# Optimization experiments

Hardware: AMD Instinct MI355X
Metric: run time of the kernel (lower is better)

## Reference

```python
import jax, jax.numpy as jnp
import numpy as np

B, T, U = 8, 200, 50
EPROJS = 512
DUNITS = 512
EMB = 512
JOINT = 512
ODIM = 1000
BLANK = 0


def setup_inputs() -> dict:
    key = jax.random.key(0)
    ks = jax.random.split(key, 16)
    s = lambda k, shape: (jax.random.normal(k, shape, jnp.float32) * 0.05)
    inp = {
        "hs_pad": jax.random.normal(ks[0], (B, T, EPROJS), jnp.float32),
        "ys_in_pad": jax.random.randint(ks[1], (B, U), 0, ODIM),
        "emb": s(ks[2], (ODIM, EMB)),
        "W_ih_0": s(ks[3], (4 * DUNITS, EMB)),
        "W_hh_0": s(ks[4], (4 * DUNITS, DUNITS)),
        "b_ih_0": s(ks[5], (4 * DUNITS,)),
        "b_hh_0": s(ks[6], (4 * DUNITS,)),
        "W_ih_1": s(ks[7], (4 * DUNITS, DUNITS)),
        "W_hh_1": s(ks[8], (4 * DUNITS, DUNITS)),
        "b_ih_1": s(ks[9], (4 * DUNITS,)),
        "b_hh_1": s(ks[10], (4 * DUNITS,)),
        "W_enc": s(ks[11], (JOINT, EPROJS)),
        "b_enc": s(ks[12], (JOINT,)),
        "W_dec": s(ks[13], (JOINT, DUNITS)),
        "W_out": s(ks[14], (ODIM, JOINT)),
        "b_out": s(ks[15], (ODIM,)),
    }
    return inp


def _lstm_cell(x, h, c, W_ih, W_hh, b_ih, b_hh):
    # torch.nn.LSTMCell, gate order i, f, g, o
    gates = x @ W_ih.T + b_ih + h @ W_hh.T + b_hh
    i, f, g, o = jnp.split(gates, 4, axis=-1)
    c_new = jax.nn.sigmoid(f) * c + jax.nn.sigmoid(i) * jnp.tanh(g)
    h_new = jax.nn.sigmoid(o) * jnp.tanh(c_new)
    return h_new, c_new


def reference(hs_pad, ys_in_pad, emb, W_ih_0, W_hh_0, b_ih_0, b_hh_0,
              W_ih_1, W_hh_1, b_ih_1, b_hh_1, W_enc, b_enc, W_dec,
              W_out, b_out):
    # embedding with padding_idx=blank -> blank row is zero
    emb_tbl = emb.at[BLANK].set(0.0)
    eys = emb_tbl[ys_in_pad]            # (B, U, EMB)

    def step(carry, ey):
        h0, c0, h1, c1 = carry
        h0, c0 = _lstm_cell(ey, h0, c0, W_ih_0, W_hh_0, b_ih_0, b_hh_0)
        h1, c1 = _lstm_cell(h0, h1, c1, W_ih_1, W_hh_1, b_ih_1, b_hh_1)
        return (h0, c0, h1, c1), h1

    z0 = jnp.zeros((hs_pad.shape[0], DUNITS), hs_pad.dtype)
    _, h_dec = jax.lax.scan(step, (z0, z0, z0, z0),
                            jnp.swapaxes(eys, 0, 1))   # (U, B, D)
    h_dec = jnp.swapaxes(h_dec, 0, 1)                  # (B, U, D)

    # joint: project first, then broadcast-add (avoids (B,T,U,Henc) expand)
    z_enc = hs_pad @ W_enc.T + b_enc                   # (B, T, J)
    z_dec = h_dec @ W_dec.T                            # (B, U, J), no bias
    z = jnp.tanh(z_enc[:, :, None, :] + z_dec[:, None, :, :])  # (B,T,U,J)
    return z @ W_out.T + b_out                         # (B, T, U, ODIM)
```

## Files before the change

kernel.cpp:

```cpp
#include <hip/hip_runtime.h>
#include <cstdint>
#include <cstddef>

#define Tsz 200
#define Usz 50
#define Kd  512
#define G4h 2048
#define OD  1000

typedef __attribute__((ext_vector_type(8))) short short8;
typedef __attribute__((ext_vector_type(4))) short s16x4;
typedef __attribute__((ext_vector_type(4))) float f32x4;

__device__ __forceinline__ unsigned short f2bf(float x) {
  union { float f; unsigned u; } v; v.f = x;
  unsigned r = v.u + 0x7FFFu + ((v.u >> 16) & 1u);
  return (unsigned short)(r >> 16);
}
__device__ __forceinline__ float bf2f(unsigned short h) {
  union { unsigned u; float f; } v; v.u = ((unsigned)h) << 16; return v.f;
}
__device__ __forceinline__ void splits(float w, short& hi, short& lo) {
  unsigned short h = f2bf(w);
  hi = (short)h;
  lo = (short)f2bf(w - bf2f(h));
}
__device__ __forceinline__ void split8(float4 f0, float4 f1, short8& hi, short8& lo) {
  float v[8] = {f0.x, f0.y, f0.z, f0.w, f1.x, f1.y, f1.z, f1.w};
  #pragma unroll
  for (int i = 0; i < 8; ++i) { short a, b2; splits(v[i], a, b2); hi[i] = a; lo[i] = b2; }
}
__device__ __forceinline__ float ftanh(float x) {
  float ax = fabsf(x);
  float t = __expf(-2.0f * ax);
  float r = (1.0f - t) / (1.0f + t);
  return copysignf(r, x);
}
__device__ __forceinline__ float sigf(float x) {
  return 1.0f / (1.0f + __expf(-x));
}
__device__ __forceinline__ void astore(unsigned* p, unsigned v) {
  __hip_atomic_store(p, v, __ATOMIC_RELAXED, __HIP_MEMORY_SCOPE_AGENT);
}
__device__ __forceinline__ void gload16(const void* g, void* l) {
  __builtin_amdgcn_global_load_lds(
      (const __attribute__((address_space(1))) void*)g,
      (__attribute__((address_space(3))) void*)l, 16, 0, 0);
}
__device__ __forceinline__ void aload4x4(const unsigned* p0, const unsigned* p1,
                                         const unsigned* p2, const unsigned* p3,
                                         uint4& r0, uint4& r1, uint4& r2, uint4& r3) {
  asm volatile(
      "global_load_dwordx4 %0, %4, off sc0 sc1\n\t"
      "global_load_dwordx4 %1, %5, off sc0 sc1\n\t"
      "global_load_dwordx4 %2, %6, off sc0 sc1\n\t"
      "global_load_dwordx4 %3, %7, off sc0 sc1\n\t"
      "s_waitcnt vmcnt(0)"
      : "=&v"(r0), "=&v"(r1), "=&v"(r2), "=&v"(r3)
      : "v"(p0), "v"(p1), "v"(p2), "v"(p3)
      : "memory");
}
__device__ __forceinline__ void aload8x4(const unsigned* p0, const unsigned* p1,
                                         const unsigned* p2, const unsigned* p3,
                                         const unsigned* q0, const unsigned* q1,
                                         const unsigned* q2, const unsigned* q3,
                                         uint4& r0, uint4& r1, uint4& r2, uint4& r3,
                                         uint4& s0, uint4& s1, uint4& s2, uint4& s3) {
  asm volatile(
      "global_load_dwordx4 %0, %8, off sc0 sc1\n\t"
      "global_load_dwordx4 %1, %9, off sc0 sc1\n\t"
      "global_load_dwordx4 %2, %10, off sc0 sc1\n\t"
      "global_load_dwordx4 %3, %11, off sc0 sc1\n\t"
      "global_load_dwordx4 %4, %12, off sc0 sc1\n\t"
      "global_load_dwordx4 %5, %13, off sc0 sc1\n\t"
      "global_load_dwordx4 %6, %14, off sc0 sc1\n\t"
      "global_load_dwordx4 %7, %15, off sc0 sc1\n\t"
      "s_waitcnt vmcnt(0)"
      : "=&v"(r0), "=&v"(r1), "=&v"(r2), "=&v"(r3),
        "=&v"(s0), "=&v"(s1), "=&v"(s2), "=&v"(s3)
      : "v"(p0), "v"(p1), "v"(p2), "v"(p3),
        "v"(q0), "v"(q1), "v"(q2), "v"(q3)
      : "memory");
}
__device__ __forceinline__ unsigned tagbad4(uint4 v, unsigned tg) {
  return ((v.x ^ tg) | (v.y ^ tg) | (v.z ^ tg) | (v.w ^ tg)) & 0xFFu;
}

__global__ __launch_bounds__(256) void k_init(unsigned* __restrict__ h0s,
                                              unsigned* __restrict__ h1s) {
  int i = blockIdx.x * 256 + threadIdx.x;
  if (i < 4096) { h0s[i] = 0u; h1s[i] = 0u; }
}

__global__ __launch_bounds__(256) void k_embed(const int* __restrict__ ys,
                                               const float* __restrict__ emb,
                                               float* __restrict__ eys) {
  int ub = blockIdx.x;
  int u = ub >> 3, b = ub & 7;
  int idx = ys[b * Usz + u];
  float* dst = eys + (size_t)ub * Kd;
  if (idx == 0) {
    for (int k = threadIdx.x; k < Kd; k += 256) dst[k] = 0.0f;
  } else {
    const float* src = emb + (size_t)idx * Kd;
    for (int k = threadIdx.x; k < Kd; k += 256) dst[k] = src[k];
  }
}

__global__ __launch_bounds__(256) void k_gemm(const float* __restrict__ A,
                                              const float* __restrict__ W,
                                              const float* __restrict__ b1,
                                              const float* __restrict__ b2,
                                              float* __restrict__ C, int N) {
  __shared__ float Al[16 * 516];
  int m0 = blockIdx.x * 16;
  int n0 = blockIdx.y * 64;
  for (int i = threadIdx.x; i < 16 * 512; i += 256) {
    int r = i >> 9, k = i & 511;
    Al[r * 516 + k] = A[(size_t)(m0 + r) * Kd + k];
  }
  __syncthreads();
  int nl = threadIdx.x & 63;
  int mg = (threadIdx.x >> 6) * 4;
  int n = n0 + nl;
  const float* Wr = W + (size_t)n * Kd;
  float acc[4] = {0.f, 0.f, 0.f, 0.f};
  #pragma unroll 4
  for (int k = 0; k < 512; k += 4) {
    float4 w = *(const float4*)(Wr + k);
    #pragma unroll
    for (int j = 0; j < 4; ++j) {
      const float* ar = &Al[(mg + j) * 516 + k];
      acc[j] += ar[0] * w.x + ar[1] * w.y + ar[2] * w.z + ar[3] * w.w;
    }
  }
  float bias = (b1 ? b1[n] : 0.0f) + (b2 ? b2[n] : 0.0f);
  #pragma unroll
  for (int j = 0; j < 4; ++j)
    C[(size_t)(m0 + mg + j) * N + n] = acc[j] + bias;
}

__global__ __launch_bounds__(256) void k_gemm_xg(const float* __restrict__ A,
                                                 const float* __restrict__ W,
                                                 const float* __restrict__ b1,
                                                 const float* __restrict__ b2,
                                                 float* __restrict__ C) {
  __shared__ float Al[16 * 516];
  int m0 = blockIdx.x * 16;
  int n0 = blockIdx.y * 64;
  for (int i = threadIdx.x; i < 16 * 512; i += 256) {
    int r = i >> 9, k = i & 511;
    Al[r * 516 + k] = A[(size_t)(m0 + r) * Kd + k];
  }
  __syncthreads();
  int nl = threadIdx.x & 63;
  int mg = (threadIdx.x >> 6) * 4;
  int n = n0 + nl;
  const float* Wr = W + (size_t)n * Kd;
  float acc[4] = {0.f, 0.f, 0.f, 0.f};
  #pragma unroll 4
  for (int k = 0; k < 512; k += 4) {
    float4 w = *(const float4*)(Wr + k);
    #pragma unroll
    for (int j = 0; j < 4; ++j) {
      const float* ar = &Al[(mg + j) * 516 + k];
      acc[j] += ar[0] * w.x + ar[1] * w.y + ar[2] * w.z + ar[3] * w.w;
    }
  }
  float bias = b1[n] + b2[n];
  int g = n >> 9, jc = n & 511;
  #pragma unroll
  for (int j = 0; j < 4; ++j) {
    int m = m0 + mg + j;
    int u = m >> 3, b = m & 7;
    C[(((size_t)u * 32 + (jc >> 4)) * 4 + g) * 128 + (jc & 15) * 8 + b] = acc[j] + bias;
  }
}

__global__ __launch_bounds__(256, 1) void k_lstm_all(
    const float* __restrict__ Whh0, const float* __restrict__ Wih1,
    const float* __restrict__ Whh1, const float* __restrict__ bih1,
    const float* __restrict__ bhh1, const float* __restrict__ xgr,
    unsigned* __restrict__ h0s, unsigned* __restrict__ h1s,
    float* __restrict__ hdec) {
  __shared__ __align__(16) unsigned short sd[34816];
  unsigned short* H0H = sd;
  unsigned short* H0L = sd + 8192;
  unsigned short* H1H = sd + 16384;
  unsigned short* H1L = sd + 24576;
  float* gsm = (float*)(sd + 32768);

  const int tid = threadIdx.x;
  const int lane = tid & 63;
  const int wv = tid >> 6;
  const int bid = blockIdx.x;
  const int kq = lane >> 4;
  const int cl = lane & 15;
  const int gg = (tid & 127) >> 1;
  const int sub = (tid & 1) << 3;
  const int swz = (gg & 7) << 4;
  const int gbase = gg << 8;
  const int tb = tid >> 7;

  if (bid < 32) {
    const int j0 = bid * 16;
    short8 whi[16], wlo[16];
    {
      const float* wr = Whh0 + ((size_t)(wv * 512 + j0 + cl)) * Kd;
      #pragma unroll
      for (int kt = 0; kt < 16; ++kt) {
        const float* p4 = wr + kt * 32 + kq * 8;
        split8(*(const float4*)p4, *(const float4*)(p4 + 4), whi[kt], wlo[kt]);
      }
    }
    float creg = 0.0f;
    const int ejl = tid & 15, eb = (tid >> 4) & 7;
    for (int p = 0; p < 50; ++p) {
      const float* xp = xgr + (((size_t)p * 32 + bid) * 4) * 128 + ejl * 8 + eb;
      float x0 = xp[0], x1 = xp[128], x2 = xp[256], x3 = xp[384];
      {
        const unsigned* bp = h0s + (size_t)p * 4096 + (tid << 2);
        uint4 v0, v1, v2, v3;
        aload4x4(bp, bp + 1024, bp + 2048, bp + 3072, v0, v1, v2, v3);
        const unsigned tg = (unsigned)p;
        for (int guard = 0; guard < (1 << 18); ++guard) {
          unsigned bad = tagbad4(v0, tg) | tagbad4(v1, tg) |
                         tagbad4(v2, tg) | tagbad4(v3, tg);
          if (!bad) break;
          __builtin_amdgcn_s_sleep(1);
          aload4x4(bp, bp + 1024, bp + 2048, bp + 3072, v0, v1, v2, v3);
        }
        unsigned uu[4][4] = {{v0.x, v0.y, v0.z, v0.w}, {v1.x, v1.y, v1.z, v1.w},
                             {v2.x, v2.y, v2.z, v2.w}, {v3.x, v3.y, v3.z, v3.w}};
        #pragma unroll
        for (int j = 0; j < 4; ++j) {
          s16x4 hv, lv;
          #pragma unroll
          for (int e = 0; e < 4; ++e) {
            short hh, ll; splits(__uint_as_float(uu[j][e]), hh, ll);
            hv[e] = hh; lv[e] = ll;
          }
          int b = j * 2 + tb;
          int off = gbase + (((b << 4) + sub) ^ swz);
          *(s16x4*)((char*)H0H + off) = hv;
          *(s16x4*)((char*)H0L + off) = lv;
        }
      }
      __syncthreads();
      f32x4 accA = {0.f, 0.f, 0.f, 0.f};
      f32x4 accB = {0.f, 0.f, 0.f, 0.f};
      f32x4 accC = {0.f, 0.f, 0.f, 0.f};
      #pragma unroll
      for (int kt = 0; kt < 16; ++kt) {
        int g = kt * 4 + kq;
        int off = (g << 8) + ((cl << 4) ^ ((g & 7) << 4));
        short8 bh = *(const short8*)((const char*)H0H + off);
        short8 bl = *(const short8*)((const char*)H0L + off);
        accA = __builtin_amdgcn_mfma_f32_16x16x32_bf16(whi[kt], bh, accA, 0, 0, 0);
        accB = __builtin_amdgcn_mfma_f32_16x16x32_bf16(wlo[kt], bh, accB, 0, 0, 0);
        accC = __builtin_amdgcn_mfma_f32_16x16x32_bf16(whi[kt], bl, accC, 0, 0, 0);
      }
      f32x4 acc = (accA + accB) + accC;
      *(f32x4*)&gsm[(wv * 16 + cl) * 16 + kq * 4] = acc;
      __syncthreads();
      if (tid < 128) {
        float g0 = gsm[(0 * 16 + eb) * 16 + ejl];
        float g1 = gsm[(1 * 16 + eb) * 16 + ejl];
        float g2 = gsm[(2 * 16 + eb) * 16 + ejl];
        float g3 = gsm[(3 * 16 + eb) * 16 + ejl];
        float gi = g0 + x0;
        float gf = g1 + x1;
        float gg2 = g2 + x2;
        float go = g3 + x3;
        float cn = sigf(gf) * creg + sigf(gi) * ftanh(gg2);
        float hn = sigf(go) * ftanh(cn);
        creg = cn;
        unsigned hv = (__float_as_uint(hn) & ~0xFFu) | (unsigned)(p + 1);
        astore(h0s + (size_t)(p + 1) * 4096 + eb * 512 + j0 + ejl, hv);
      }
      __syncthreads();
    }
  } else {
    const int j0 = (bid - 32) * 8;
    const int mt = wv & 1, kh = wv >> 1;
    short8 wihh[8], wihl[8], whhh[8], whhl[8];
    {
      const int g = mt * 2 + (cl >> 3), jl = cl & 7;
      const float* wr0 = Wih1 + ((size_t)(g * 512 + j0 + jl)) * Kd;
      const float* wr1 = Whh1 + ((size_t)(g * 512 + j0 + jl)) * Kd;
      #pragma unroll
      for (int k2 = 0; k2 < 8; ++k2) {
        int kt = kh * 8 + k2;
        const float* p0 = wr0 + kt * 32 + kq * 8;
        const float* p1 = wr1 + kt * 32 + kq * 8;
        split8(*(const float4*)p0, *(const float4*)(p0 + 4), wihh[k2], wihl[k2]);
        split8(*(const float4*)p1, *(const float4*)(p1 + 4), whhh[k2], whhl[k2]);
      }
    }
    float creg = 0.0f;
    const int ejl = tid & 7, eb = (tid >> 3) & 7;
    float bs0 = bih1[0 * 512 + j0 + ejl] + bhh1[0 * 512 + j0 + ejl];
    float bs1 = bih1[1 * 512 + j0 + ejl] + bhh1[1 * 512 + j0 + ejl];
    float bs2 = bih1[2 * 512 + j0 + ejl] + bhh1[2 * 512 + j0 + ejl];
    float bs3 = bih1[3 * 512 + j0 + ejl] + bhh1[3 * 512 + j0 + ejl];
    for (int p = 1; p <= 50; ++p) {
      {
        const unsigned* bp0 = h0s + (size_t)p * 4096 + (tid << 2);
        const unsigned* bp1 = h1s + (size_t)(p - 1) * 4096 + (tid << 2);
        uint4 v0, v1, v2, v3, w0, w1, w2, w3;
        aload8x4(bp0, bp0 + 1024, bp0 + 2048, bp0 + 3072,
                 bp1, bp1 + 1024, bp1 + 2048, bp1 + 3072,
                 v0, v1, v2, v3, w0, w1, w2, w3);
        const unsigned tg0 = (unsigned)p, tg1 = (unsigned)(p - 1);
        for (int guard = 0; guard < (1 << 18); ++guard) {
          unsigned bad = tagbad4(v0, tg0) | tagbad4(v1, tg0) |
                         tagbad4(v2, tg0) | tagbad4(v3, tg0) |
                         tagbad4(w0, tg1) | tagbad4(w1, tg1) |
                         tagbad4(w2, tg1) | tagbad4(w3, tg1);
          if (!bad) break;
          __builtin_amdgcn_s_sleep(1);
          aload8x4(bp0, bp0 + 1024, bp0 + 2048, bp0 + 3072,
                   bp1, bp1 + 1024, bp1 + 2048, bp1 + 3072,
                   v0, v1, v2, v3, w0, w1, w2, w3);
        }
        unsigned uu[4][4] = {{v0.x, v0.y, v0.z, v0.w}, {v1.x, v1.y, v1.z, v1.w},
                             {v2.x, v2.y, v2.z, v2.w}, {v3.x, v3.y, v3.z, v3.w}};
        unsigned tt[4][4] = {{w0.x, w0.y, w0.z, w0.w}, {w1.x, w1.y, w1.z, w1.w},
                             {w2.x, w2.y, w2.z, w2.w}, {w3.x, w3.y, w3.z, w3.w}};
        #pragma unroll
        for (int j = 0; j < 4; ++j) {
          s16x4 hv, lv, hw, lw;
          #pragma unroll
          for (int e = 0; e < 4; ++e) {
            short hh, ll;
            splits(__uint_as_float(uu[j][e]), hh, ll); hv[e] = hh; lv[e] = ll;
            splits(__uint_as_float(tt[j][e]), hh, ll); hw[e] = hh; lw[e] = ll;
          }
          int b = j * 2 + tb;
          int off = gbase + (((b << 4) + sub) ^ swz);
          *(s16x4*)((char*)H0H + off) = hv;
          *(s16x4*)((char*)H0L + off) = lv;
          *(s16x4*)((char*)H1H + off) = hw;
          *(s16x4*)((char*)H1L + off) = lw;
        }
      }
      __syncthreads();
      f32x4 q0 = {0.f,0.f,0.f,0.f}, q1 = {0.f,0.f,0.f,0.f}, q2 = {0.f,0.f,0.f,0.f};
      f32x4 q3 = {0.f,0.f,0.f,0.f}, q4 = {0.f,0.f,0.f,0.f}, q5 = {0.f,0.f,0.f,0.f};
      #pragma unroll
      for (int k2 = 0; k2 < 8; ++k2) {
        int kt = kh * 8 + k2;
        int g = kt * 4 + kq;
        int off = (g << 8) + ((cl << 4) ^ ((g & 7) << 4));
        short8 b0h = *(const short8*)((const char*)H0H + off);
        short8 b0l = *(const short8*)((const char*)H0L + off);
        short8 b1h = *(const short8*)((const char*)H1H + off);
        short8 b1l = *(const short8*)((const char*)H1L + off);
        q0 = __builtin_amdgcn_mfma_f32_16x16x32_bf16(wihh[k2], b0h, q0, 0, 0, 0);
        q1 = __builtin_amdgcn_mfma_f32_16x16x32_bf16(wihl[k2], b0h, q1, 0, 0, 0);
        q2 = __builtin_amdgcn_mfma_f32_16x16x32_bf16(wihh[k2], b0l, q2, 0, 0, 0);
        q3 = __builtin_amdgcn_mfma_f32_16x16x32_bf16(whhh[k2], b1h, q3, 0, 0, 0);
        q4 = __builtin_amdgcn_mfma_f32_16x16x32_bf16(whhl[k2], b1h, q4, 0, 0, 0);
        q5 = __builtin_amdgcn_mfma_f32_16x16x32_bf16(whhh[k2], b1l, q5, 0, 0, 0);
      }
      f32x4 acc = ((q0 + q1) + (q2 + q3)) + (q4 + q5);
      *(f32x4*)&gsm[(wv * 16 + cl) * 16 + kq * 4] = acc;
      __syncthreads();
      if (tid < 64) {
        float gv[4];
        #pragma unroll
        for (int g = 0; g < 4; ++g) {
          int mtg = g >> 1, r = (g & 1) * 8 + ejl;
          gv[g] = gsm[(mtg * 16 + eb) * 16 + r] + gsm[((2 + mtg) * 16 + eb) * 16 + r];
        }
        float gi = gv[0] + bs0, gf = gv[1] + bs1, gg2 = gv[2] + bs2, go = gv[3] + bs3;
        float cn = sigf(gf) * creg + sigf(gi) * ftanh(gg2);
        float hn = sigf(go) * ftanh(cn);
        creg = cn;
        int jg = j0 + ejl;
        unsigned hv = (__float_as_uint(hn) & ~0xFFu) | (unsigned)p;
        astore(h1s + (size_t)p * 4096 + eb * 512 + jg, hv);
        hdec[((size_t)eb * Usz + (p - 1)) * Kd + jg] = __uint_as_float(hv);
      }
      __syncthreads();
    }
  }
}

__global__ __launch_bounds__(256) void k_wcvt(const float* __restrict__ W,
                                              unsigned short* __restrict__ Wb) {
  int idx = blockIdx.x * 256 + threadIdx.x;
  int n = idx >> 6, chunk = idx & 63;
  short8 v;
  if (n < OD) {
    const float* src = W + (size_t)n * Kd + chunk * 8;
    #pragma unroll
    for (int j = 0; j < 8; ++j) v[j] = (short)f2bf(src[j]);
  } else {
    #pragma unroll
    for (int j = 0; j < 8; ++j) v[j] = 0;
  }
  int tile = n >> 5, srow = n & 31;
  size_t off = (size_t)tile * 32768 + srow * 1024 + ((chunk * 16) ^ ((srow & 7) << 4));
  *(short8*)((char*)Wb + off) = v;
}

__global__ __launch_bounds__(256) void k_joint(const float* __restrict__ zenc,
                                               const float* __restrict__ zdec,
                                               const unsigned short* __restrict__ Wb,
                                               const float* __restrict__ bout,
                                               float* __restrict__ out) {
  __shared__ __align__(16) unsigned short Blds[2 * 16384];
  const int lane = threadIdx.x & 63;
  const int wv = threadIdx.x >> 6;
  const int kgrp = lane >> 4;
  const int rl = lane & 15;

  for (int item = blockIdx.x; item < 1250; item += 512) {
    const int rbase = item * 64 + wv * 16;

    short8 a[16];
    {
      int row = rbase + rl;
      int u = row % Usz;
      int bt = row / Usz;
      const float* ze = zenc + (size_t)bt * Kd;
      const float* zd = zdec + (size_t)((bt / Tsz) * Usz + u) * Kd;
      #pragma unroll
      for (int kk = 0; kk < 16; ++kk) {
        int k0 = kk * 32 + kgrp * 8;
        float4 e0 = *(const float4*)(ze + k0);
        float4 e1 = *(const float4*)(ze + k0 + 4);
        float4 d0 = *(const float4*)(zd + k0);
        float4 d1 = *(const float4*)(zd + k0 + 4);
        short8 tt;
        tt[0] = (short)f2bf(ftanh(e0.x + d0.x));
        tt[1] = (short)f2bf(ftanh(e0.y + d0.y));
        tt[2] = (short)f2bf(ftanh(e0.z + d0.z));
        tt[3] = (short)f2bf(ftanh(e0.w + d0.w));
        tt[4] = (short)f2bf(ftanh(e1.x + d1.x));
        tt[5] = (short)f2bf(ftanh(e1.y + d1.y));
        tt[6] = (short)f2bf(ftanh(e1.z + d1.z));
        tt[7] = (short)f2bf(ftanh(e1.w + d1.w));
        a[kk] = tt;
      }
    }

    #pragma unroll
    for (int i = 0; i < 8; ++i) {
      int o = (i * 4 + wv) * 1024;
      gload16((const char*)Wb + o + lane * 16, (char*)Blds + o);
    }
    __syncthreads();

    int cur = 0;
    for (int it = 0; it < 32; ++it) {
      if (it < 31) {
        const char* g = (const char*)Wb + (size_t)(it + 1) * 32768;
        char* l = (char*)Blds + (cur ^ 1) * 32768;
        #pragma unroll
        for (int i = 0; i < 8; ++i) {
          int o = (i * 4 + wv) * 1024;
          gload16(g + o + lane * 16, l + o);
        }
      }
      const char* bufc = (const char*)Blds + cur * 32768;
      int n0 = it * 32;
      f32x4 acc0 = {0.f, 0.f, 0.f, 0.f};
      f32x4 acc1 = {0.f, 0.f, 0.f, 0.f};
      #pragma unroll
      for (int kk = 0; kk < 16; ++kk) {
        int c = kk * 4 + kgrp;
        int b0 = ((c * 16) ^ ((rl & 7) << 4)) + rl * 1024;
        int b1 = ((c * 16) ^ ((rl & 7) << 4)) + (rl + 16) * 1024;
        short8 bf0 = *(const short8*)(bufc + b0);
        short8 bf1 = *(const short8*)(bufc + b1);
        acc0 = __builtin_amdgcn_mfma_f32_16x16x32_bf16(a[kk], bf0, acc0, 0, 0, 0);
        acc1 = __builtin_amdgcn_mfma_f32_16x16x32_bf16(a[kk], bf1, acc1, 0, 0, 0);
      }
      #pragma unroll
      for (int nt = 0; nt < 2; ++nt) {
        int n = n0 + nt * 16 + rl;
        if (n < OD) {
          float bo = bout[n];
          const f32x4& A0 = nt ? acc1 : acc0;
          size_t r0 = (size_t)(rbase + kgrp * 4) * OD + n;
          #pragma unroll
          for (int j = 0; j < 4; ++j)
            out[r0 + (size_t)j * OD] = A0[j] + bo;
        }
      }
      __syncthreads();
      cur ^= 1;
    }
  }
}

extern "C" void kernel_launch(void* const* d_in, const int* in_sizes, int n_in,
                              void* d_out, int out_size, void* d_ws, size_t ws_size,
                              hipStream_t stream) {
  const float* hs   = (const float*)d_in[0];
  const int*   ys   = (const int*)d_in[1];
  const float* emb  = (const float*)d_in[2];
  const float* Wih0 = (const float*)d_in[3];
  const float* Whh0 = (const float*)d_in[4];
  const float* bih0 = (const float*)d_in[5];
  const float* bhh0 = (const float*)d_in[6];
  const float* Wih1 = (const float*)d_in[7];
  const float* Whh1 = (const float*)d_in[8];
  const float* bih1 = (const float*)d_in[9];
  const float* bhh1 = (const float*)d_in[10];
  const float* Wenc = (const float*)d_in[11];
  const float* benc = (const float*)d_in[12];
  const float* Wdec = (const float*)d_in[13];
  const float* Wout = (const float*)d_in[14];
  const float* bout = (const float*)d_in[15];
  float* out = (float*)d_out;

  float* ws   = (float*)d_ws;
  float* eys  = ws;
  float* xgr  = ws + 204800;
  float* zenc = ws + 1024000;
  float* zdec = ws + 1843200;
  float* hdec = ws + 2048000;
  unsigned short* Wb = (unsigned short*)(ws + 2252800);
  unsigned* h0s = (unsigned*)(ws + 2514944);
  unsigned* h1s = (unsigned*)(ws + 2723840);

  k_init<<<16, 256, 0, stream>>>(h0s, h1s);
  k_embed<<<400, 256, 0, stream>>>(ys, emb, eys);
  k_gemm_xg<<<dim3(25, 32), 256, 0, stream>>>(eys, Wih0, bih0, bhh0, xgr);
  k_gemm<<<dim3(100, 8), 256, 0, stream>>>(hs, Wenc, benc, nullptr, zenc, 512);
  k_wcvt<<<256, 256, 0, stream>>>(Wout, Wb);
  k_lstm_all<<<96, 256, 0, stream>>>(Whh0, Wih1, Whh1, bih1, bhh1, xgr,
                                     h0s, h1s, hdec);
  k_gemm<<<dim3(25, 8), 256, 0, stream>>>(hdec, Wdec, nullptr, nullptr, zdec, 512);
  k_joint<<<512, 256, 0, stream>>>(zenc, zdec, Wb, bout, out);
}
```

Before: 437.2 us.

## Merge prep kernels into one launch and retune joint pipeline sync

```diff
diff --git a/kernel.cpp b/kernel.cpp
--- a/kernel.cpp
+++ b/kernel.cpp
@@ -86,31 +86,116 @@
   return ((v.x ^ tg) | (v.y ^ tg) | (v.z ^ tg) | (v.w ^ tg)) & 0xFFu;
 }
 
-__global__ __launch_bounds__(256) void k_init(unsigned* __restrict__ h0s,
-                                              unsigned* __restrict__ h1s) {
-  int i = blockIdx.x * 256 + threadIdx.x;
-  if (i < 4096) { h0s[i] = 0u; h1s[i] = 0u; }
-}
-
-__global__ __launch_bounds__(256) void k_embed(const int* __restrict__ ys,
-                                               const float* __restrict__ emb,
-                                               float* __restrict__ eys) {
-  int ub = blockIdx.x;
-  int u = ub >> 3, b = ub & 7;
-  int idx = ys[b * Usz + u];
-  float* dst = eys + (size_t)ub * Kd;
-  if (idx == 0) {
-    for (int k = threadIdx.x; k < Kd; k += 256) dst[k] = 0.0f;
-  } else {
-    const float* src = emb + (size_t)idx * Kd;
-    for (int k = threadIdx.x; k < Kd; k += 256) dst[k] = src[k];
+__global__ __launch_bounds__(256) void k_prep(
+    const int* __restrict__ ys, const float* __restrict__ emb,
+    const float* __restrict__ Wih0, const float* __restrict__ bih0,
+    const float* __restrict__ bhh0, const float* __restrict__ hs,
+    const float* __restrict__ Wenc, const float* __restrict__ benc,
+    const float* __restrict__ Wout,
+    unsigned* __restrict__ h0s, unsigned* __restrict__ h1s,
+    unsigned short* __restrict__ Wb, float* __restrict__ zenc,
+    float* __restrict__ xgr) {
+  __shared__ float Al[16 * 516];
+  __shared__ int idxs[16];
+  const int bid = blockIdx.x;
+  const int tid = threadIdx.x;
+
+  if (bid < 16) {
+    int i = bid * 256 + tid;
+    if (i < 4096) { h0s[i] = 0u; h1s[i] = 0u; }
+    return;
+  }
+  if (bid < 272) {
+    int idx = (bid - 16) * 256 + tid;
+    int n = idx >> 6, chunk = idx & 63;
+    short8 v;
+    if (n < OD) {
+      const float* src = Wout + (size_t)n * Kd + chunk * 8;
+      #pragma unroll
+      for (int j = 0; j < 8; ++j) v[j] = (short)f2bf(src[j]);
+    } else {
+      #pragma unroll
+      for (int j = 0; j < 8; ++j) v[j] = 0;
+    }
+    int tile = n >> 5, srow = n & 31;
+    size_t off = (size_t)tile * 32768 + srow * 1024 +
+                 ((chunk * 16) ^ ((srow & 7) << 4));
+    *(short8*)((char*)Wb + off) = v;
+    return;
+  }
+  if (bid < 1072) {
+    int q = bid - 272;
+    int m0 = (q % 100) * 16;
+    int n0 = (q / 100) * 64;
+    for (int i = tid; i < 16 * 512; i += 256) {
+      int r = i >> 9, k = i & 511;
+      Al[r * 516 + k] = hs[(size_t)(m0 + r) * Kd + k];
+    }
+    __syncthreads();
+    int nl = tid & 63;
+    int mg = (tid >> 6) * 4;
+    int n = n0 + nl;
+    const float* Wr = Wenc + (size_t)n * Kd;
+    float acc[4] = {0.f, 0.f, 0.f, 0.f};
+    #pragma unroll 4
+    for (int k = 0; k < 512; k += 4) {
+      float4 w = *(const float4*)(Wr + k);
+      #pragma unroll
+      for (int j = 0; j < 4; ++j) {
+        const float* ar = &Al[(mg + j) * 516 + k];
+        acc[j] += ar[0] * w.x + ar[1] * w.y + ar[2] * w.z + ar[3] * w.w;
+      }
+    }
+    float bias = benc[n];
+    #pragma unroll
+    for (int j = 0; j < 4; ++j)
+      zenc[(size_t)(m0 + mg + j) * 512 + n] = acc[j] + bias;
+    return;
+  }
+  {
+    int q = bid - 1072;
+    int m0 = (q % 25) * 16;
+    int n0 = (q / 25) * 64;
+    if (tid < 16) {
+      int m = m0 + tid;
+      int u = m >> 3, b = m & 7;
+      idxs[tid] = ys[b * Usz + u];
+    }
+    __syncthreads();
+    for (int i = tid; i < 16 * 512; i += 256) {
+      int r = i >> 9, k = i & 511;
+      int idx = idxs[r];
+      Al[r * 516 + k] = (idx == 0) ? 0.0f : emb[(size_t)idx * Kd + k];
+    }
+    __syncthreads();
+    int nl = tid & 63;
+    int mg = (tid >> 6) * 4;
+    int n = n0 + nl;
+    const float* Wr = Wih0 + (size_t)n * Kd;
+    float acc[4] = {0.f, 0.f, 0.f, 0.f};
+    #pragma unroll 4
+    for (int k = 0; k < 512; k += 4) {
+      float4 w = *(const float4*)(Wr + k);
+      #pragma unroll
+      for (int j = 0; j < 4; ++j) {
+        const float* ar = &Al[(mg + j) * 516 + k];
+        acc[j] += ar[0] * w.x + ar[1] * w.y + ar[2] * w.z + ar[3] * w.w;
+      }
+    }
+    float bias = bih0[n] + bhh0[n];
+    int g = n >> 9, jc = n & 511;
+    #pragma unroll
+    for (int j = 0; j < 4; ++j) {
+      int m = m0 + mg + j;
+      int u = m >> 3, b = m & 7;
+      xgr[(((size_t)u * 32 + (jc >> 4)) * 4 + g) * 128 + (jc & 15) * 8 + b] =
+          acc[j] + bias;
+    }
   }
 }
 
 __global__ __launch_bounds__(256) void k_gemm(const float* __restrict__ A,
                                               const float* __restrict__ W,
-                                              const float* __restrict__ b1,
-                                              const float* __restrict__ b2,
                                               float* __restrict__ C, int N) {
   __shared__ float Al[16 * 516];
   int m0 = blockIdx.x * 16;
@@ -134,47 +219,9 @@
       acc[j] += ar[0] * w.x + ar[1] * w.y + ar[2] * w.z + ar[3] * w.w;
     }
   }
-  float bias = (b1 ? b1[n] : 0.0f) + (b2 ? b2[n] : 0.0f);
   #pragma unroll
   for (int j = 0; j < 4; ++j)
-    C[(size_t)(m0 + mg + j) * N + n] = acc[j] + bias;
-}
-
-__global__ __launch_bounds__(256) void k_gemm_xg(const float* __restrict__ A,
-                                                 const float* __restrict__ W,
-                                                 const float* __restrict__ b1,
-                                                 const float* __restrict__ b2,
-                                                 float* __restrict__ C) {
-  __shared__ float Al[16 * 516];
-  int m0 = blockIdx.x * 16;
-  int n0 = blockIdx.y * 64;
-  for (int i = threadIdx.x; i < 16 * 512; i += 256) {
-    int r = i >> 9, k = i & 511;
-    Al[r * 516 + k] = A[(size_t)(m0 + r) * Kd + k];
-  }
-  __syncthreads();
-  int nl = threadIdx.x & 63;
-  int mg = (threadIdx.x >> 6) * 4;
-  int n = n0 + nl;
-  const float* Wr = W + (size_t)n * Kd;
-  float acc[4] = {0.f, 0.f, 0.f, 0.f};
-  #pragma unroll 4
-  for (int k = 0; k < 512; k += 4) {
-    float4 w = *(const float4*)(Wr + k);
-    #pragma unroll
-    for (int j = 0; j < 4; ++j) {
-      const float* ar = &Al[(mg + j) * 516 + k];
-      acc[j] += ar[0] * w.x + ar[1] * w.y + ar[2] * w.z + ar[3] * w.w;
-    }
-  }
-  float bias = b1[n] + b2[n];
-  int g = n >> 9, jc = n & 511;
-  #pragma unroll
-  for (int j = 0; j < 4; ++j) {
-    int m = m0 + mg + j;
-    int u = m >> 3, b = m & 7;
-    C[(((size_t)u * 32 + (jc >> 4)) * 4 + g) * 128 + (jc & 15) * 8 + b] = acc[j] + bias;
-  }
+    C[(size_t)(m0 + mg + j) * N + n] = acc[j];
 }
 
 __global__ __launch_bounds__(256, 1) void k_lstm_all(
@@ -387,24 +434,6 @@
   }
 }
 
-__global__ __launch_bounds__(256) void k_wcvt(const float* __restrict__ W,
-                                              unsigned short* __restrict__ Wb) {
-  int idx = blockIdx.x * 256 + threadIdx.x;
-  int n = idx >> 6, chunk = idx & 63;
-  short8 v;
-  if (n < OD) {
-    const float* src = W + (size_t)n * Kd + chunk * 8;
-    #pragma unroll
-    for (int j = 0; j < 8; ++j) v[j] = (short)f2bf(src[j]);
-  } else {
-    #pragma unroll
-    for (int j = 0; j < 8; ++j) v[j] = 0;
-  }
-  int tile = n >> 5, srow = n & 31;
-  size_t off = (size_t)tile * 32768 + srow * 1024 + ((chunk * 16) ^ ((srow & 7) << 4));
-  *(short8*)((char*)Wb + off) = v;
-}
-
 __global__ __launch_bounds__(256) void k_joint(const float* __restrict__ zenc,
                                                const float* __restrict__ zdec,
                                                const unsigned short* __restrict__ Wb,
@@ -415,84 +444,89 @@
   const int wv = threadIdx.x >> 6;
   const int kgrp = lane >> 4;
   const int rl = lane & 15;
-
-  for (int item = blockIdx.x; item < 1250; item += 512) {
-    const int rbase = item * 64 + wv * 16;
-
-    short8 a[16];
-    {
-      int row = rbase + rl;
-      int u = row % Usz;
-      int bt = row / Usz;
-      const float* ze = zenc + (size_t)bt * Kd;
-      const float* zd = zdec + (size_t)((bt / Tsz) * Usz + u) * Kd;
-      #pragma unroll
-      for (int kk = 0; kk < 16; ++kk) {
-        int k0 = kk * 32 + kgrp * 8;
-        float4 e0 = *(const float4*)(ze + k0);
-        float4 e1 = *(const float4*)(ze + k0 + 4);
-        float4 d0 = *(const float4*)(zd + k0);
-        float4 d1 = *(const float4*)(zd + k0 + 4);
-        short8 tt;
-        tt[0] = (short)f2bf(ftanh(e0.x + d0.x));
-        tt[1] = (short)f2bf(ftanh(e0.y + d0.y));
-        tt[2] = (short)f2bf(ftanh(e0.z + d0.z));
-        tt[3] = (short)f2bf(ftanh(e0.w + d0.w));
-        tt[4] = (short)f2bf(ftanh(e1.x + d1.x));
-        tt[5] = (short)f2bf(ftanh(e1.y + d1.y));
-        tt[6] = (short)f2bf(ftanh(e1.z + d1.z));
-        tt[7] = (short)f2bf(ftanh(e1.w + d1.w));
-        a[kk] = tt;
-      }
-    }
-
+  const int rbase = blockIdx.x * 64 + wv * 16;
+
+  short8 a[16];
+  {
+    int row = rbase + rl;
+    int u = row % Usz;
+    int bt = row / Usz;
+    const float* ze = zenc + (size_t)bt * Kd;
+    const float* zd = zdec + (size_t)((bt / Tsz) * Usz + u) * Kd;
     #pragma unroll
-    for (int i = 0; i < 8; ++i) {
-      int o = (i * 4 + wv) * 1024;
-      gload16((const char*)Wb + o + lane * 16, (char*)Blds + o);
-    }
-    __syncthreads();
-
-    int cur = 0;
-    for (int it = 0; it < 32; ++it) {
-      if (it < 31) {
-        const char* g = (const char*)Wb + (size_t)(it + 1) * 32768;
-        char* l = (char*)Blds + (cur ^ 1) * 32768;
+    for (int kk = 0; kk < 16; ++kk) {
+      int k0 = kk * 32 + kgrp * 8;
+      float4 e0 = *(const float4*)(ze + k0);
+      float4 e1 = *(const float4*)(ze + k0 + 4);
+      float4 d0 = *(const float4*)(zd + k0);
+      float4 d1 = *(const float4*)(zd + k0 + 4);
+      short8 tt;
+      tt[0] = (short)f2bf(ftanh(e0.x + d0.x));
+      tt[1] = (short)f2bf(ftanh(e0.y + d0.y));
+      tt[2] = (short)f2bf(ftanh(e0.z + d0.z));
+      tt[3] = (short)f2bf(ftanh(e0.w + d0.w));
+      tt[4] = (short)f2bf(ftanh(e1.x + d1.x));
+      tt[5] = (short)f2bf(ftanh(e1.y + d1.y));
+      tt[6] = (short)f2bf(ftanh(e1.z + d1.z));
+      tt[7] = (short)f2bf(ftanh(e1.w + d1.w));
+      a[kk] = tt;
+    }
+  }
+
+  #pragma unroll
+  for (int i = 0; i < 8; ++i) {
+    int o = (i * 4 + wv) * 1024;
+    gload16((const char*)Wb + o + lane * 16, (char*)Blds + o);
+  }
+  asm volatile("s_waitcnt vmcnt(0)" ::: "memory");
+  __builtin_amdgcn_s_barrier();
+  __builtin_amdgcn_sched_barrier(0);
+
+  int cur = 0;
+  for (int it = 0; it < 32; ++it) {
+    if (it < 31) {
+      const char* g = (const char*)Wb + (size_t)(it + 1) * 32768;
+      char* l = (char*)Blds + (cur ^ 1) * 32768;
+      #pragma unroll
+      for (int i = 0; i < 8; ++i) {
+        int o = (i * 4 + wv) * 1024;
+        gload16(g + o + lane * 16, l + o);
+      }
+      __builtin_amdgcn_sched_barrier(0);
+    }
+    const char* bufc = (const char*)Blds + cur * 32768;
+    int n0 = it * 32;
+    f32x4 acc0 = {0.f, 0.f, 0.f, 0.f};
+    f32x4 acc1 = {0.f, 0.f, 0.f, 0.f};
+    #pragma unroll
+    for (int kk = 0; kk < 16; ++kk) {
+      int c = kk * 4 + kgrp;
+      int b0 = ((c * 16) ^ ((rl & 7) << 4)) + rl * 1024;
+      int b1 = ((c * 16) ^ ((rl & 7) << 4)) + (rl + 16) * 1024;
+      short8 bf0 = *(const short8*)(bufc + b0);
+      short8 bf1 = *(const short8*)(bufc + b1);
+      acc0 = __builtin_amdgcn_mfma_f32_16x16x32_bf16(a[kk], bf0, acc0, 0, 0, 0);
+      acc1 = __builtin_amdgcn_mfma_f32_16x16x32_bf16(a[kk], bf1, acc1, 0, 0, 0);
+    }
+    #pragma unroll
+    for (int nt = 0; nt < 2; ++nt) {
+      int n = n0 + nt * 16 + rl;
+      if (n < OD) {
+        float bo = bout[n];
+        const f32x4& A0 = nt ? acc1 : acc0;
+        size_t r0 = (size_t)(rbase + kgrp * 4) * OD + n;
         #pragma unroll
-        for (int i = 0; i < 8; ++i) {
-          int o = (i * 4 + wv) * 1024;
-          gload16(g + o + lane * 16, l + o);
-        }
-      }
-      const char* bufc = (const char*)Blds + cur * 32768;
-      int n0 = it * 32;
-      f32x4 acc0 = {0.f, 0.f, 0.f, 0.f};
-      f32x4 acc1 = {0.f, 0.f, 0.f, 0.f};
-      #pragma unroll
-      for (int kk = 0; kk < 16; ++kk) {
-        int c = kk * 4 + kgrp;
-        int b0 = ((c * 16) ^ ((rl & 7) << 4)) + rl * 1024;
-        int b1 = ((c * 16) ^ ((rl & 7) << 4)) + (rl + 16) * 1024;
-        short8 bf0 = *(const short8*)(bufc + b0);
-        short8 bf1 = *(const short8*)(bufc + b1);
-        acc0 = __builtin_amdgcn_mfma_f32_16x16x32_bf16(a[kk], bf0, acc0, 0, 0, 0);
-        acc1 = __builtin_amdgcn_mfma_f32_16x16x32_bf16(a[kk], bf1, acc1, 0, 0, 0);
-      }
-      #pragma unroll
-      for (int nt = 0; nt < 2; ++nt) {
-        int n = n0 + nt * 16 + rl;
-        if (n < OD) {
-          float bo = bout[n];
-          const f32x4& A0 = nt ? acc1 : acc0;
-          size_t r0 = (size_t)(rbase + kgrp * 4) * OD + n;
-          #pragma unroll
-          for (int j = 0; j < 4; ++j)
-            out[r0 + (size_t)j * OD] = A0[j] + bo;
-        }
-      }
-      __syncthreads();
-      cur ^= 1;
-    }
+        for (int j = 0; j < 4; ++j)
+          out[r0 + (size_t)j * OD] = A0[j] + bo;
+      }
+    }
+    if (it < 31) {
+      __builtin_amdgcn_sched_barrier(0);
+      asm volatile("s_waitcnt vmcnt(8)" ::: "memory");
+      __builtin_amdgcn_s_barrier();
+      __builtin_amdgcn_sched_barrier(0);
+    }
+    cur ^= 1;
   }
 }
 
@@ -518,7 +552,6 @@
   float* out = (float*)d_out;
 
   float* ws   = (float*)d_ws;
-  float* eys  = ws;
   float* xgr  = ws + 204800;
   float* zenc = ws + 1024000;
   float* zdec = ws + 1843200;
@@ -527,13 +560,10 @@
   unsigned* h0s = (unsigned*)(ws + 2514944);
   unsigned* h1s = (unsigned*)(ws + 2723840);
 
-  k_init<<<16, 256, 0, stream>>>(h0s, h1s);
-  k_embed<<<400, 256, 0, stream>>>(ys, emb, eys);
-  k_gemm_xg<<<dim3(25, 32), 256, 0, stream>>>(eys, Wih0, bih0, bhh0, xgr);
-  k_gemm<<<dim3(100, 8), 256, 0, stream>>>(hs, Wenc, benc, nullptr, zenc, 512);
-  k_wcvt<<<256, 256, 0, stream>>>(Wout, Wb);
+  k_prep<<<1872, 256, 0, stream>>>(ys, emb, Wih0, bih0, bhh0, hs, Wenc, benc,
+                                   Wout, h0s, h1s, Wb, zenc, xgr);
   k_lstm_all<<<96, 256, 0, stream>>>(Whh0, Wih1, Whh1, bih1, bhh1, xgr,
                                      h0s, h1s, hdec);
-  k_gemm<<<dim3(25, 8), 256, 0, stream>>>(hdec, Wdec, nullptr, nullptr, zdec, 512);
-  k_joint<<<512, 256, 0, stream>>>(zenc, zdec, Wb, bout, out);
-}
+  k_gemm<<<dim3(25, 8), 256, 0, stream>>>(hdec, Wdec, zdec, 512);
+  k_joint<<<1250, 256, 0, stream>>>(zenc, zdec, Wb, bout, out);
+}
```

Result: faster. 406.8 us (-6.9%).
